# Kernel tuning notes

Measured on AMD Instinct MI355X. Metric: run time of the kernel, lower is better.

## Reference

```python
import jax, jax.numpy as jnp
import numpy as np

# ---- constants from conf ----
DT = 0.01
INIT_TAU = 0.5
MIN_TAU = 0.1
VTH = 1.0
VREST = 0.0
SLOPE = 25.0  # snntorch surrogate.fast_sigmoid default slope
IN, H1, H2, OUT = 700, 1024, 1024, 20
T, B = 100, 256

# fast-sigmoid surrogate: heaviside forward, 1/(1+slope|x|)^2 backward
@jax.custom_vjp
def spike_fn(x):
    return (x > 0).astype(x.dtype)

def _spike_fwd(x):
    return spike_fn(x), x

def _spike_bwd(x, g):
    return (g / (1.0 + SLOPE * jnp.abs(x)) ** 2,)

spike_fn.defvjp(_spike_fwd, _spike_bwd)

def lif_step(v, cur, w_tau):
    # per-neuron trainable time constant: tau = min_tau + sigmoid(w)
    tau = MIN_TAU + jax.nn.sigmoid(w_tau)
    v_new = v + (DT / tau) * (VREST - v + cur)
    s = spike_fn(v_new - VTH)
    v_reset = v_new * (1.0 - s) + VREST * s  # reset-to-zero mechanism
    return s, v_new, v_reset

def setup_inputs() -> dict:
    key = jax.random.key(0)
    ks = jax.random.split(key, 7)
    w_tau0 = float(np.log((INIT_TAU - MIN_TAU) / (1.0 - (INIT_TAU - MIN_TAU))))
    def lin(k, fan_in, fan_out):
        bound = 1.0 / np.sqrt(fan_in)
        kw, kb = jax.random.split(k)
        W = jax.random.uniform(kw, (fan_out, fan_in), jnp.float32, -bound, bound)
        b = jax.random.uniform(kb, (fan_out,), jnp.float32, -bound, bound)
        return W, b
    W1, b1 = lin(ks[0], IN, H1)
    W2, b2 = lin(ks[1], H1, H2)
    W3, b3 = lin(ks[2], H2, OUT)
    return {
        "s": jax.random.uniform(ks[3], (T, B, IN), jnp.float32),
        "W1": W1, "b1": b1, "wt1": jnp.full((H1,), w_tau0, jnp.float32),
        "W2": W2, "b2": b2, "wt2": jnp.full((H2,), w_tau0, jnp.float32),
        "W3": W3, "b3": b3, "wt3": jnp.full((OUT,), w_tau0, jnp.float32),
    }

def reference(s, W1, b1, wt1, W2, b2, wt2, W3, b3, wt3):
    Bq = s.shape[1]
    v0 = (jnp.full((Bq, H1), VREST, s.dtype),
          jnp.full((Bq, H2), VREST, s.dtype),
          jnp.full((Bq, OUT), VREST, s.dtype))

    def step(carry, st):
        v1, v2, v3 = carry
        s1, _, v1r = lif_step(v1, st @ W1.T + b1, wt1)
        s2, _, v2r = lif_step(v2, s1 @ W2.T + b2, wt2)
        s3, v3n, v3r = lif_step(v3, s2 @ W3.T + b3, wt3)
        return (v1r, v2r, v3r), (s3, v3n)

    _, (out_s, out_v) = jax.lax.scan(step, v0, s)
    return out_s, out_v  # [T,B,OUT] spikes and pre-reset membrane
```

## Files before the change

kernel.cpp:

```cpp
#include <hip/hip_runtime.h>

#define DT 0.01f
#define MIN_TAU 0.1f
#define VTH 1.0f
#define IN_DIM 700
#define H1 1024
#define H2 1024
#define OUT_DIM 20
#define T_STEPS 100
#define BATCH 256
#define M_ROWS (T_STEPS * BATCH)
#define KB_CNT 22
#define MT_CNT 1600
#define NT_CNT 64

typedef unsigned short u16;
typedef __attribute__((ext_vector_type(4))) float f32x4;
typedef __attribute__((ext_vector_type(8))) short short8;

__device__ __forceinline__ float bf2f(u16 u){ return __uint_as_float(((unsigned)u) << 16); }
__device__ __forceinline__ u16 f2bf(float f){
    unsigned x = __float_as_uint(f);
    return (u16)((x + 0x7fffu + ((x >> 16) & 1u)) >> 16);
}
template<bool ISBF>
__device__ __forceinline__ float ld1(const void* p, size_t i){
    return ISBF ? bf2f(((const u16*)p)[i]) : ((const float*)p)[i];
}

template<bool ISBF>
__global__ __launch_bounds__(256) void prep_tile(
    const void* __restrict__ Sraw, const void* __restrict__ W1raw,
    const void* __restrict__ b1raw, const void* __restrict__ wt1raw,
    u16* __restrict__ Stil, u16* __restrict__ Wtil, float* __restrict__ B1f)
{
    const u16* wt1u = (const u16*)wt1raw;
    if ((wt1u[0] == wt1u[1]) != ISBF) return;

    int u = blockIdx.x * 256 + threadIdx.x;
    const int SU = MT_CNT * KB_CNT * 64;
    const int WU = NT_CNT * KB_CNT * 64;
    if (u >= SU + WU){
        int i = u - SU - WU;
        B1f[i] = ld1<ISBF>(b1raw, i);
        return;
    }
    const void* src;
    u16* dst;
    int tile, lo;
    if (u < SU){ tile = u >> 6; lo = u & 63; src = Sraw;  dst = Stil; }
    else { int uu = u - SU; tile = uu >> 6; lo = uu & 63; src = W1raw; dst = Wtil; }
    const int rt = tile / KB_CNT, kb = tile - rt * KB_CNT;
    const int lr = lo >> 2, lg = lo & 3;
    const int row = rt * 16 + lr;
    const int k0 = kb * 32 + lg * 8;

    u16 out[8];
    if (k0 + 7 < IN_DIM){
        if (ISBF){
            const u16* p = (const u16*)src + (size_t)row * IN_DIM + k0;
            ushort4 q0 = *(const ushort4*)p, q1 = *(const ushort4*)(p + 4);
            out[0]=q0.x; out[1]=q0.y; out[2]=q0.z; out[3]=q0.w;
            out[4]=q1.x; out[5]=q1.y; out[6]=q1.z; out[7]=q1.w;
        } else {
            const float* p = (const float*)src + (size_t)row * IN_DIM + k0;
            float4 f0 = *(const float4*)p, f1 = *(const float4*)(p + 4);
            out[0]=f2bf(f0.x); out[1]=f2bf(f0.y); out[2]=f2bf(f0.z); out[3]=f2bf(f0.w);
            out[4]=f2bf(f1.x); out[5]=f2bf(f1.y); out[6]=f2bf(f1.z); out[7]=f2bf(f1.w);
        }
    } else {
        #pragma unroll
        for (int j = 0; j < 8; ++j){
            int k = k0 + j;
            out[j] = (k < IN_DIM) ? (ISBF ? ((const u16*)src)[(size_t)row * IN_DIM + k]
                                          : f2bf(((const float*)src)[(size_t)row * IN_DIM + k]))
                                  : (u16)0;
        }
    }
    *(short8*)&dst[(size_t)tile * 512 + lo * 8] = *(short8*)&out[0];
}

__global__ __launch_bounds__(512) void gemm256(
    const u16* __restrict__ Stil, const u16* __restrict__ Wtil,
    const float* __restrict__ B1f, u16* __restrict__ CUR1)
{
    __shared__ u16 Lb[2][24 * 512];
    const int bid = blockIdx.x;
    const int swz = (bid & 7) * 100 + (bid >> 3);
    const int mB = swz >> 3, nB = swz & 7;
    const int tid = threadIdx.x;
    const int lane = tid & 63, wv = tid >> 6;
    const int lr = lane & 15, lg = lane >> 4;
    const int loff = lr * 32 + lg * 8;
    const int wm = wv >> 1, wn = wv & 1;

    const int tgrp = tid >> 6;
    const int l16o = (tid & 63) * 8;
    const u16* pA0 = Stil + (size_t)(mB * 16 +     tgrp) * KB_CNT * 512 + l16o;
    const u16* pA1 = Stil + (size_t)(mB * 16 + 8 + tgrp) * KB_CNT * 512 + l16o;
    const u16* pB0 = Wtil + (size_t)(nB * 8  +     tgrp) * KB_CNT * 512 + l16o;
    const int d0 = tgrp * 512 + l16o;
    const int d1 = (8 + tgrp) * 512 + l16o;
    const int d2 = (16 + tgrp) * 512 + l16o;

    const int m0g = mB * 256 + wm * 64, n0g = nB * 128 + wn * 64;
    float bias[4];
    #pragma unroll
    for (int nf = 0; nf < 4; ++nf) bias[nf] = B1f[n0g + nf * 16 + lr];

    f32x4 acc[4][4];
    #pragma unroll
    for (int i = 0; i < 4; ++i)
        #pragma unroll
        for (int j = 0; j < 4; ++j) acc[i][j] = (f32x4){0.f, 0.f, 0.f, 0.f};

    short8 sA0 = *(const short8*)pA0;
    short8 sA1 = *(const short8*)pA1;
    short8 sB0 = *(const short8*)pB0;
    *(short8*)&Lb[0][d0] = sA0;
    *(short8*)&Lb[0][d1] = sA1;
    *(short8*)&Lb[0][d2] = sB0;
    __syncthreads();

    int cur = 0;
    #pragma unroll 1
    for (int kb = 0; kb < KB_CNT; ++kb){
        const bool more = (kb + 1) < KB_CNT;
        if (more){
            sA0 = *(const short8*)(pA0 + (kb + 1) * 512);
            sA1 = *(const short8*)(pA1 + (kb + 1) * 512);
            sB0 = *(const short8*)(pB0 + (kb + 1) * 512);
        }
        short8 af[4], bf[4];
        #pragma unroll
        for (int mf = 0; mf < 4; ++mf)
            af[mf] = *(const short8*)&Lb[cur][(wm * 4 + mf) * 512 + loff];
        #pragma unroll
        for (int nf = 0; nf < 4; ++nf)
            bf[nf] = *(const short8*)&Lb[cur][(16 + wn * 4 + nf) * 512 + loff];
        #pragma unroll
        for (int mf = 0; mf < 4; ++mf)
            #pragma unroll
            for (int nf = 0; nf < 4; ++nf)
                acc[mf][nf] = __builtin_amdgcn_mfma_f32_16x16x32_bf16(
                    af[mf], bf[nf], acc[mf][nf], 0, 0, 0);
        if (more){
            *(short8*)&Lb[cur ^ 1][d0] = sA0;
            *(short8*)&Lb[cur ^ 1][d1] = sA1;
            *(short8*)&Lb[cur ^ 1][d2] = sB0;
        }
        __syncthreads();
        cur ^= 1;
    }

    #pragma unroll
    for (int mf = 0; mf < 4; ++mf)
        #pragma unroll
        for (int nf = 0; nf < 4; ++nf)
            #pragma unroll
            for (int r = 0; r < 4; ++r)
                CUR1[(size_t)(m0g + mf*16 + lg*4 + r) * H1 + (n0g + nf*16 + lr)]
                    = f2bf(acc[mf][nf][r] + bias[nf]);
}

template<bool ISBF>
__global__ __launch_bounds__(64, 1) void scan_wave(
    const u16* __restrict__ CUR1,
    const void* __restrict__ wt1raw,
    const void* __restrict__ W2raw, const void* __restrict__ b2raw,
    const void* __restrict__ wt2raw,const void* __restrict__ W3raw,
    const void* __restrict__ b3raw, const void* __restrict__ wt3raw,
    void* __restrict__ outraw)
{
    const u16* wt1u = (const u16*)wt1raw;
    if ((wt1u[0] == wt1u[1]) != ISBF) return;

    const int b = blockIdx.x, lane = threadIdx.x;
    const int n0 = lane * 16;

    float v1[16], v2[16], kk1[16], kk2[16], b2f[16];
    #pragma unroll
    for (int r = 0; r < 16; ++r){
        kk1[r] = DT / (MIN_TAU + 1.f / (1.f + expf(-ld1<ISBF>(wt1raw, n0 + r))));
        kk2[r] = DT / (MIN_TAU + 1.f / (1.f + expf(-ld1<ISBF>(wt2raw, n0 + r))));
        b2f[r] = ld1<ISBF>(b2raw, n0 + r);
        v1[r] = 0.f; v2[r] = 0.f;
    }
    float v3 = 0.f, kk3 = 0.f, b3f = 0.f;
    if (lane < OUT_DIM){
        kk3 = DT / (MIN_TAU + 1.f / (1.f + expf(-ld1<ISBF>(wt3raw, lane))));
        b3f = ld1<ISBF>(b3raw, lane);
    }
    const size_t TBO = (size_t)T_STEPS * BATCH * OUT_DIM;
    const u16* cbase = CUR1 + (size_t)b * H1 + n0;
    const size_t tstride = (size_t)BATCH * H1;

    float rec_v[5];
    float rec_s[5];

    auto ldc = [&](int t, short8* dst){
        if (t < T_STEPS){
            const u16* p = cbase + (size_t)t * tstride;
            dst[0] = *(const short8*)p;
            dst[1] = *(const short8*)(p + 8);
        } else {
            dst[0] = (short8){0,0,0,0,0,0,0,0};
            dst[1] = (short8){0,0,0,0,0,0,0,0};
        }
    };

    auto do_step = [&](int s, short8 c0, short8 c1){
        #pragma unroll
        for (int r = 0; r < 16; ++r){
            u16 cu = (u16)(r < 8 ? c0[r] : c1[r - 8]);
            v1[r] = v1[r] + kk1[r] * (bf2f(cu) - v1[r]);
        }
        float mx1 = v1[0];
        #pragma unroll
        for (int r = 1; r < 16; ++r) mx1 = fmaxf(mx1, v1[r]);

        float cur3 = b3f;
        if (__any(mx1 > VTH)){
            unsigned m1 = 0u;
            #pragma unroll
            for (int r = 0; r < 16; ++r){
                bool sp = v1[r] > VTH;
                v1[r] = sp ? 0.f : v1[r];
                m1 |= sp ? (1u << r) : 0u;
            }
            unsigned long long bal1 = __ballot((int)(m1 != 0u));
            float cur2[16];
            #pragma unroll
            for (int r = 0; r < 16; ++r) cur2[r] = b2f[r];
            unsigned long long bb = bal1;
            while (bb){
                int L = __ffsll(bb) - 1; bb &= bb - 1;
                unsigned mk = __shfl(m1, L);
                while (mk){
                    int j = L * 16 + __ffs(mk) - 1; mk &= mk - 1;
                    #pragma unroll
                    for (int r = 0; r < 16; ++r)
                        cur2[r] += ld1<ISBF>(W2raw, (size_t)(n0 + r) * H1 + j);
                }
            }
            unsigned m2 = 0u;
            #pragma unroll
            for (int r = 0; r < 16; ++r){
                float vn = v2[r] + kk2[r] * (cur2[r] - v2[r]);
                bool sp = vn > VTH;
                v2[r] = sp ? 0.f : vn;
                m2 |= sp ? (1u << r) : 0u;
            }
            unsigned long long bal2 = __ballot((int)(m2 != 0u));
            unsigned long long b2b = bal2;
            while (b2b){
                int L = __ffsll(b2b) - 1; b2b &= b2b - 1;
                unsigned mk = __shfl(m2, L);
                while (mk){
                    int j = L * 16 + __ffs(mk) - 1; mk &= mk - 1;
                    float w = (lane < OUT_DIM)
                            ? ld1<ISBF>(W3raw, (size_t)lane * H2 + j) : 0.f;
                    cur3 += w;
                }
            }
        } else {
            #pragma unroll
            for (int r = 0; r < 16; ++r)
                v2[r] = v2[r] + kk2[r] * (b2f[r] - v2[r]);
            float mx2 = v2[0];
            #pragma unroll
            for (int r = 1; r < 16; ++r) mx2 = fmaxf(mx2, v2[r]);
            if (__any(mx2 > VTH)){
                unsigned m2 = 0u;
                #pragma unroll
                for (int r = 0; r < 16; ++r){
                    bool sp = v2[r] > VTH;
                    v2[r] = sp ? 0.f : v2[r];
                    m2 |= sp ? (1u << r) : 0u;
                }
                unsigned long long bal2 = __ballot((int)(m2 != 0u));
                unsigned long long b2b = bal2;
                while (b2b){
                    int L = __ffsll(b2b) - 1; b2b &= b2b - 1;
                    unsigned mk = __shfl(m2, L);
                    while (mk){
                        int j = L * 16 + __ffs(mk) - 1; mk &= mk - 1;
                        float w = (lane < OUT_DIM)
                                ? ld1<ISBF>(W3raw, (size_t)lane * H2 + j) : 0.f;
                        cur3 += w;
                    }
                }
            }
        }

        float vn3 = v3 + kk3 * (cur3 - v3);
        bool sp3 = vn3 > VTH;
        rec_s[s] = sp3 ? 1.f : 0.f;
        rec_v[s] = vn3;
        v3 = sp3 ? 0.f : vn3;
    };

    auto flush = [&](int tb){
        if (lane < OUT_DIM){
            #pragma unroll
            for (int s = 0; s < 5; ++s){
                int t = tb + s;
                size_t o = ((size_t)t * BATCH + b) * OUT_DIM + lane;
                if (ISBF){
                    u16* ob = (u16*)outraw;
                    ob[o] = (rec_s[s] != 0.f) ? (u16)0x3F80 : (u16)0;
                    ob[TBO + o] = f2bf(rec_v[s]);
                } else {
                    float* of = (float*)outraw;
                    of[o] = rec_s[s];
                    of[TBO + o] = rec_v[s];
                }
            }
        }
    };

    short8 pA[5][2], pB[5][2];
    #pragma unroll
    for (int s = 0; s < 5; ++s) ldc(s, pA[s]);

    #pragma unroll 1
    for (int g2 = 0; g2 < 10; ++g2){
        const int tb = g2 * 10;
        #pragma unroll
        for (int s = 0; s < 5; ++s) ldc(tb + 5 + s, pB[s]);
        #pragma unroll
        for (int s = 0; s < 5; ++s) do_step(s, pA[s][0], pA[s][1]);
        flush(tb);
        #pragma unroll
        for (int s = 0; s < 5; ++s) ldc(tb + 10 + s, pA[s]);
        #pragma unroll
        for (int s = 0; s < 5; ++s) do_step(s, pB[s][0], pB[s][1]);
        flush(tb + 5);
    }
}

template<bool ISBF>
__global__ __launch_bounds__(256) void gemm_cur1(
    const void* __restrict__ Sraw, const void* __restrict__ W1raw,
    const void* __restrict__ wt1raw, u16* __restrict__ CUR1)
{
    const u16* wt1u = (const u16*)wt1raw;
    if ((wt1u[0] == wt1u[1]) != ISBF) return;

    __shared__ u16 lds[2][2][128][40];
    const int tid = threadIdx.x;
    const int n0 = blockIdx.x * 128;
    const int m0 = blockIdx.y * 128;
    const int row = tid >> 1, half = tid & 1;
    const int lane = tid & 63, wv = tid >> 6;
    const int lr = lane & 15, lg = lane >> 4;
    const int wm = wv >> 1, wn = wv & 1;

    float4  fa[4], fb[4];
    ushort4 ha[4], hb[4];

    auto load_seg = [&](const void* base, int grow, int kb, float4* fr, ushort4* hr){
        const int cg0 = kb * 32 + half * 16;
        #pragma unroll
        for (int q = 0; q < 4; ++q){
            const int cg = cg0 + q * 4;
            if (ISBF){
                const u16* p = (const u16*)base + (size_t)grow * IN_DIM + cg;
                ushort4 v = make_ushort4(0,0,0,0);
                if (cg + 3 < IN_DIM) v = *(const ushort4*)p;
                else {
                    if (cg     < IN_DIM) v.x = p[0];
                    if (cg + 1 < IN_DIM) v.y = p[1];
                    if (cg + 2 < IN_DIM) v.z = p[2];
                    if (cg + 3 < IN_DIM) v.w = p[3];
                }
                hr[q] = v;
            } else {
                const float* p = (const float*)base + (size_t)grow * IN_DIM + cg;
                float4 f = make_float4(0,0,0,0);
                if (cg + 3 < IN_DIM) f = *(const float4*)p;
                else {
                    if (cg     < IN_DIM) f.x = p[0];
                    if (cg + 1 < IN_DIM) f.y = p[1];
                    if (cg + 2 < IN_DIM) f.z = p[2];
                    if (cg + 3 < IN_DIM) f.w = p[3];
                }
                fr[q] = f;
            }
        }
    };
    auto load_ab = [&](int kb){
        load_seg(Sraw,  m0 + row, kb, fa, ha);
        load_seg(W1raw, n0 + row, kb, fb, hb);
    };
    auto cvt_store = [&](int buf){
        u16 ta[16], tb[16];
        #pragma unroll
        for (int q = 0; q < 4; ++q){
            if (ISBF){
                ta[q*4+0]=ha[q].x; ta[q*4+1]=ha[q].y; ta[q*4+2]=ha[q].z; ta[q*4+3]=ha[q].w;
                tb[q*4+0]=hb[q].x; tb[q*4+1]=hb[q].y; tb[q*4+2]=hb[q].z; tb[q*4+3]=hb[q].w;
            } else {
                ta[q*4+0]=f2bf(fa[q].x); ta[q*4+1]=f2bf(fa[q].y);
                ta[q*4+2]=f2bf(fa[q].z); ta[q*4+3]=f2bf(fa[q].w);
                tb[q*4+0]=f2bf(fb[q].x); tb[q*4+1]=f2bf(fb[q].y);
                tb[q*4+2]=f2bf(fb[q].z); tb[q*4+3]=f2bf(fb[q].w);
            }
        }
        *(short8*)&lds[0][buf][row][half*16    ] = *(short8*)&ta[0];
        *(short8*)&lds[0][buf][row][half*16 + 8] = *(short8*)&ta[8];
        *(short8*)&lds[1][buf][row][half*16    ] = *(short8*)&tb[0];
        *(short8*)&lds[1][buf][row][half*16 + 8] = *(short8*)&tb[8];
    };

    f32x4 acc[4][4];
    #pragma unroll
    for (int i = 0; i < 4; ++i)
        #pragma unroll
        for (int j = 0; j < 4; ++j) acc[i][j] = (f32x4){0.f,0.f,0.f,0.f};

    load_ab(0);
    cvt_store(0);
    __syncthreads();

    for (int kb = 0; kb < 22; ++kb){
        const int cur = kb & 1;
        const bool more = (kb + 1) < 22;
        if (more) load_ab(kb + 1);

        short8 afr[4], bfr[4];
        #pragma unroll
        for (int mf = 0; mf < 4; ++mf)
            afr[mf] = *(const short8*)&lds[0][cur][wm*64 + mf*16 + lr][lg*8];
        #pragma unroll
        for (int nf = 0; nf < 4; ++nf)
            bfr[nf] = *(const short8*)&lds[1][cur][wn*64 + nf*16 + lr][lg*8];
        #pragma unroll
        for (int mf = 0; mf < 4; ++mf)
            #pragma unroll
            for (int nf = 0; nf < 4; ++nf)
                acc[mf][nf] = __builtin_amdgcn_mfma_f32_16x16x32_bf16(
                    afr[mf], bfr[nf], acc[mf][nf], 0, 0, 0);

        if (more) cvt_store(cur ^ 1);
        __syncthreads();
    }

    u16 (*Cep)[136] = (u16(*)[136])&lds[0][0][0][0];
    #pragma unroll
    for (int mf = 0; mf < 4; ++mf)
        #pragma unroll
        for (int nf = 0; nf < 4; ++nf)
            #pragma unroll
            for (int r = 0; r < 4; ++r)
                Cep[wm*64 + mf*16 + lg*4 + r][wn*64 + nf*16 + lr] = f2bf(acc[mf][nf][r]);
    __syncthreads();
    #pragma unroll
    for (int q = 0; q < 8; ++q){
        int idx = q * 256 + tid;
        int r = idx >> 4, c = (idx & 15) * 8;
        *(short8*)&CUR1[(size_t)(m0 + r) * H1 + n0 + c] = *(short8*)&Cep[r][c];
    }
}

template<bool ISBF>
__global__ __launch_bounds__(256) void scan_cur(
    const u16* __restrict__ CUR1,
    const void* __restrict__ b1raw, const void* __restrict__ wt1raw,
    const void* __restrict__ W2raw, const void* __restrict__ b2raw,
    const void* __restrict__ wt2raw,const void* __restrict__ W3raw,
    const void* __restrict__ b3raw, const void* __restrict__ wt3raw,
    void* __restrict__ outraw)
{
    const u16* wt1u = (const u16*)wt1raw;
    if ((wt1u[0] == wt1u[1]) != ISBF) return;

    const int b = blockIdx.x, tid = threadIdx.x;
    __shared__ __align__(16) unsigned mask1[2][32], mask2[2][32];
    __shared__ __align__(16) unsigned wflag1[2][4], wflag2[2][4];

    float v1[4] = {0,0,0,0}, v2[4] = {0,0,0,0};
    float kk1[4], kk2[4], b1f[4], b2f[4];
    #pragma unroll
    for (int c = 0; c < 4; ++c){
        int n = tid * 4 + c;
        kk1[c] = DT / (MIN_TAU + 1.f / (1.f + expf(-ld1<ISBF>(wt1raw, n))));
        kk2[c] = DT / (MIN_TAU + 1.f / (1.f + expf(-ld1<ISBF>(wt2raw, n))));
        b1f[c] = ld1<ISBF>(b1raw, n);
        b2f[c] = ld1<ISBF>(b2raw, n);
    }
    float v3 = 0.f, kk3 = 0.f, b3f = 0.f;
    if (tid < OUT_DIM){
        kk3 = DT / (MIN_TAU + 1.f / (1.f + expf(-ld1<ISBF>(wt3raw, tid))));
        b3f = ld1<ISBF>(b3raw, tid);
    }
    const size_t TBO = (size_t)T_STEPS * BATCH * OUT_DIM;

    if (tid < 32){ mask1[0][tid] = 0u; mask2[0][tid] = 0u; }
    if (tid < 4){ wflag1[0][tid] = 0u; wflag2[0][tid] = 0u; }

    auto ld_cur = [&](int t) -> ushort4 {
        if (t < T_STEPS)
            return *(const ushort4*)&CUR1[((size_t)t * BATCH + b) * H1 + tid * 4];
        return make_ushort4(0, 0, 0, 0);
    };

    auto do_step = [&](int t, ushort4 cu){
        const int p = t & 1;
        unsigned nib = 0u;
        u16 ca[4] = {cu.x, cu.y, cu.z, cu.w};
        #pragma unroll
        for (int c = 0; c < 4; ++c){
            float cur1 = bf2f(ca[c]) + b1f[c];
            float vn = v1[c] + kk1[c] * (cur1 - v1[c]);
            bool sp = vn > VTH;
            v1[c] = sp ? 0.f : vn;
            nib |= sp ? (1u << c) : 0u;
        }
        if (nib) atomicOr(&mask1[p][tid >> 3], nib << ((tid * 4) & 31));
        bool wany1 = __any((int)(nib != 0u));
        if ((tid & 63) == 0) wflag1[p][tid >> 6] = wany1 ? 1u : 0u;
        __syncthreads();

        uint4 f1 = *(const uint4*)&wflag1[p][0];
        float cur2[4] = {b2f[0], b2f[1], b2f[2], b2f[3]};
        if (f1.x | f1.y | f1.z | f1.w){
            for (int w = 0; w < 32; ++w){
                unsigned bits = mask1[p][w];
                while (bits){
                    int j = (w << 5) + __ffs(bits) - 1;
                    bits &= bits - 1;
                    #pragma unroll
                    for (int c = 0; c < 4; ++c)
                        cur2[c] += ld1<ISBF>(W2raw, (size_t)(tid * 4 + c) * H1 + j);
                }
            }
        }
        unsigned nib2 = 0u;
        #pragma unroll
        for (int c = 0; c < 4; ++c){
            float vn = v2[c] + kk2[c] * (cur2[c] - v2[c]);
            bool sp = vn > VTH;
            v2[c] = sp ? 0.f : vn;
            nib2 |= sp ? (1u << c) : 0u;
        }
        if (nib2) atomicOr(&mask2[p][tid >> 3], nib2 << ((tid * 4) & 31));
        bool wany2 = __any((int)(nib2 != 0u));
        if ((tid & 63) == 0) wflag2[p][tid >> 6] = wany2 ? 1u : 0u;
        if (tid >= 128 && tid < 160) mask1[p ^ 1][tid - 128] = 0u;
        if (tid >= 160 && tid < 164) wflag1[p ^ 1][tid - 160] = 0u;
        __syncthreads();

        if (tid < OUT_DIM){
            uint4 f2 = *(const uint4*)&wflag2[p][0];
            float cur3 = b3f;
            if (f2.x | f2.y | f2.z | f2.w){
                for (int w = 0; w < 32; ++w){
                    unsigned bits = mask2[p][w];
                    while (bits){
                        int j = (w << 5) + __ffs(bits) - 1;
                        bits &= bits - 1;
                        cur3 += ld1<ISBF>(W3raw, (size_t)tid * H2 + j);
                    }
                }
            }
            float vn = v3 + kk3 * (cur3 - v3);
            bool sp = vn > VTH;
            size_t o = ((size_t)t * BATCH + b) * OUT_DIM + tid;
            if (ISBF){
                u16* ob = (u16*)outraw;
                ob[o] = sp ? (u16)0x3F80 : (u16)0;
                ob[TBO + o] = f2bf(vn);
            } else {
                float* of = (float*)outraw;
                of[o] = sp ? 1.f : 0.f;
                of[TBO + o] = vn;
            }
            v3 = sp ? 0.f : vn;
        }
        if (tid >= 32 && tid < 64) mask2[p ^ 1][tid - 32] = 0u;
        if (tid >= 64 && tid < 68) wflag2[p ^ 1][tid - 64] = 0u;
        __syncthreads();
    };

    ushort4 pfA[10], pfB[10];
    #pragma unroll
    for (int s = 0; s < 10; ++s) pfA[s] = ld_cur(s);
    __syncthreads();

    #pragma unroll 1
    for (int g2 = 0; g2 < 5; ++g2){
        const int tb = g2 * 20;
        #pragma unroll
        for (int s = 0; s < 10; ++s) pfB[s] = ld_cur(tb + 10 + s);
        #pragma unroll
        for (int s = 0; s < 10; ++s) do_step(tb + s, pfA[s]);
        #pragma unroll
        for (int s = 0; s < 10; ++s) pfA[s] = ld_cur(tb + 20 + s);
        #pragma unroll
        for (int s = 0; s < 10; ++s) do_step(tb + 10 + s, pfB[s]);
    }
}

extern "C" void kernel_launch(void* const* d_in, const int* in_sizes, int n_in,
                              void* d_out, int out_size, void* d_ws, size_t ws_size,
                              hipStream_t stream)
{
    (void)in_sizes; (void)n_in; (void)out_size;
    const size_t STIL_B = (size_t)MT_CNT * KB_CNT * 512 * 2;
    const size_t WTIL_B = (size_t)NT_CNT * KB_CNT * 512 * 2;
    const size_t B1F_B  = 4096;
    const size_t CUR1_B = (size_t)M_ROWS * H1 * 2;
    const size_t NEED_T1 = STIL_B + WTIL_B + B1F_B + CUR1_B;

    if (ws_size >= NEED_T1){
        u16*   Stil = (u16*)d_ws;
        u16*   Wtil = (u16*)((char*)d_ws + STIL_B);
        float* B1f  = (float*)((char*)d_ws + STIL_B + WTIL_B);
        u16*   CUR1 = (u16*)((char*)d_ws + STIL_B + WTIL_B + B1F_B);
        const int units = (MT_CNT + NT_CNT) * KB_CNT * 64 + 1024;
        hipLaunchKernelGGL(prep_tile<false>, dim3(units / 256), dim3(256), 0, stream,
                           d_in[0], d_in[1], d_in[2], d_in[3], Stil, Wtil, B1f);
        hipLaunchKernelGGL(prep_tile<true>,  dim3(units / 256), dim3(256), 0, stream,
                           d_in[0], d_in[1], d_in[2], d_in[3], Stil, Wtil, B1f);
        hipLaunchKernelGGL(gemm256, dim3(800), dim3(512), 0, stream,
                           Stil, Wtil, B1f, CUR1);
        hipLaunchKernelGGL(scan_wave<false>, dim3(BATCH), dim3(64), 0, stream,
                           CUR1, d_in[3], d_in[4], d_in[5], d_in[6],
                           d_in[7], d_in[8], d_in[9], d_out);
        hipLaunchKernelGGL(scan_wave<true>,  dim3(BATCH), dim3(64), 0, stream,
                           CUR1, d_in[3], d_in[4], d_in[5], d_in[6],
                           d_in[7], d_in[8], d_in[9], d_out);
    } else if (ws_size >= CUR1_B){
        u16* CUR1 = (u16*)d_ws;
        hipLaunchKernelGGL(gemm_cur1<false>, dim3(8, 200), dim3(256), 0, stream,
                           d_in[0], d_in[1], d_in[3], CUR1);
        hipLaunchKernelGGL(gemm_cur1<true>,  dim3(8, 200), dim3(256), 0, stream,
                           d_in[0], d_in[1], d_in[3], CUR1);
        hipLaunchKernelGGL(scan_cur<false>, dim3(BATCH), dim3(256), 0, stream,
                           CUR1, d_in[2], d_in[3], d_in[4], d_in[5], d_in[6],
                           d_in[7], d_in[8], d_in[9], d_out);
        hipLaunchKernelGGL(scan_cur<true>,  dim3(BATCH), dim3(256), 0, stream,
                           CUR1, d_in[2], d_in[3], d_in[4], d_in[5], d_in[6],
                           d_in[7], d_in[8], d_in[9], d_out);
    }
}
```

Measured before the change: 105.5 us.

## Merge dtype-templated launches, make LDS fragment reads contiguous, deepen GEMM prefetch

```diff
diff --git a/kernel.cpp b/kernel.cpp
--- a/kernel.cpp
+++ b/kernel.cpp
@@ -23,26 +23,28 @@
     unsigned x = __float_as_uint(f);
     return (u16)((x + 0x7fffu + ((x >> 16) & 1u)) >> 16);
 }
+__device__ __forceinline__ float ldr(bool isbf, const void* p, size_t i){
+    return isbf ? bf2f(((const u16*)p)[i]) : ((const float*)p)[i];
+}
 template<bool ISBF>
 __device__ __forceinline__ float ld1(const void* p, size_t i){
     return ISBF ? bf2f(((const u16*)p)[i]) : ((const float*)p)[i];
 }
 
-template<bool ISBF>
 __global__ __launch_bounds__(256) void prep_tile(
     const void* __restrict__ Sraw, const void* __restrict__ W1raw,
     const void* __restrict__ b1raw, const void* __restrict__ wt1raw,
     u16* __restrict__ Stil, u16* __restrict__ Wtil, float* __restrict__ B1f)
 {
     const u16* wt1u = (const u16*)wt1raw;
-    if ((wt1u[0] == wt1u[1]) != ISBF) return;
+    const bool isbf = (wt1u[0] == wt1u[1]);
 
     int u = blockIdx.x * 256 + threadIdx.x;
     const int SU = MT_CNT * KB_CNT * 64;
     const int WU = NT_CNT * KB_CNT * 64;
     if (u >= SU + WU){
         int i = u - SU - WU;
-        B1f[i] = ld1<ISBF>(b1raw, i);
+        B1f[i] = ldr(isbf, b1raw, i);
         return;
     }
     const void* src;
@@ -51,13 +53,13 @@
     if (u < SU){ tile = u >> 6; lo = u & 63; src = Sraw;  dst = Stil; }
     else { int uu = u - SU; tile = uu >> 6; lo = uu & 63; src = W1raw; dst = Wtil; }
     const int rt = tile / KB_CNT, kb = tile - rt * KB_CNT;
-    const int lr = lo >> 2, lg = lo & 3;
+    const int lr = lo & 15, lg = lo >> 4;
     const int row = rt * 16 + lr;
     const int k0 = kb * 32 + lg * 8;
 
     u16 out[8];
     if (k0 + 7 < IN_DIM){
-        if (ISBF){
+        if (isbf){
             const u16* p = (const u16*)src + (size_t)row * IN_DIM + k0;
             ushort4 q0 = *(const ushort4*)p, q1 = *(const ushort4*)(p + 4);
             out[0]=q0.x; out[1]=q0.y; out[2]=q0.z; out[3]=q0.w;
@@ -72,7 +74,7 @@
         #pragma unroll
         for (int j = 0; j < 8; ++j){
             int k = k0 + j;
-            out[j] = (k < IN_DIM) ? (ISBF ? ((const u16*)src)[(size_t)row * IN_DIM + k]
+            out[j] = (k < IN_DIM) ? (isbf ? ((const u16*)src)[(size_t)row * IN_DIM + k]
                                           : f2bf(((const float*)src)[(size_t)row * IN_DIM + k]))
                                   : (u16)0;
         }
@@ -91,7 +93,7 @@
     const int tid = threadIdx.x;
     const int lane = tid & 63, wv = tid >> 6;
     const int lr = lane & 15, lg = lane >> 4;
-    const int loff = lr * 32 + lg * 8;
+    const int loff = lane * 8;
     const int wm = wv >> 1, wn = wv & 1;
 
     const int tgrp = tid >> 6;
@@ -114,43 +116,61 @@
         #pragma unroll
         for (int j = 0; j < 4; ++j) acc[i][j] = (f32x4){0.f, 0.f, 0.f, 0.f};
 
-    short8 sA0 = *(const short8*)pA0;
-    short8 sA1 = *(const short8*)pA1;
-    short8 sB0 = *(const short8*)pB0;
-    *(short8*)&Lb[0][d0] = sA0;
-    *(short8*)&Lb[0][d1] = sA1;
-    *(short8*)&Lb[0][d2] = sB0;
+    short8 eA0 = *(const short8*)pA0;
+    short8 eA1 = *(const short8*)pA1;
+    short8 eB0 = *(const short8*)pB0;
+    *(short8*)&Lb[0][d0] = eA0;
+    *(short8*)&Lb[0][d1] = eA1;
+    *(short8*)&Lb[0][d2] = eB0;
+    short8 oA0 = *(const short8*)(pA0 + 512);
+    short8 oA1 = *(const short8*)(pA1 + 512);
+    short8 oB0 = *(const short8*)(pB0 + 512);
     __syncthreads();
 
-    int cur = 0;
-    #pragma unroll 1
-    for (int kb = 0; kb < KB_CNT; ++kb){
-        const bool more = (kb + 1) < KB_CNT;
-        if (more){
-            sA0 = *(const short8*)(pA0 + (kb + 1) * 512);
-            sA1 = *(const short8*)(pA1 + (kb + 1) * 512);
-            sB0 = *(const short8*)(pB0 + (kb + 1) * 512);
-        }
+    auto compute = [&](int buf){
         short8 af[4], bf[4];
         #pragma unroll
         for (int mf = 0; mf < 4; ++mf)
-            af[mf] = *(const short8*)&Lb[cur][(wm * 4 + mf) * 512 + loff];
+            af[mf] = *(const short8*)&Lb[buf][(wm * 4 + mf) * 512 + loff];
         #pragma unroll
         for (int nf = 0; nf < 4; ++nf)
-            bf[nf] = *(const short8*)&Lb[cur][(16 + wn * 4 + nf) * 512 + loff];
+            bf[nf] = *(const short8*)&Lb[buf][(16 + wn * 4 + nf) * 512 + loff];
         #pragma unroll
         for (int mf = 0; mf < 4; ++mf)
             #pragma unroll
             for (int nf = 0; nf < 4; ++nf)
                 acc[mf][nf] = __builtin_amdgcn_mfma_f32_16x16x32_bf16(
                     af[mf], bf[nf], acc[mf][nf], 0, 0, 0);
-        if (more){
-            *(short8*)&Lb[cur ^ 1][d0] = sA0;
-            *(short8*)&Lb[cur ^ 1][d1] = sA1;
-            *(short8*)&Lb[cur ^ 1][d2] = sB0;
-        }
+    };
+
+    #pragma unroll 1
+    for (int kb = 0; kb < KB_CNT; kb += 2){
+        const bool m2 = (kb + 2) < KB_CNT;
+        if (m2){
+            eA0 = *(const short8*)(pA0 + (kb + 2) * 512);
+            eA1 = *(const short8*)(pA1 + (kb + 2) * 512);
+            eB0 = *(const short8*)(pB0 + (kb + 2) * 512);
+        }
+        compute(0);
+        *(short8*)&Lb[1][d0] = oA0;
+        *(short8*)&Lb[1][d1] = oA1;
+        *(short8*)&Lb[1][d2] = oB0;
         __syncthreads();
-        cur ^= 1;
+
+        if (m2){
+            if ((kb + 3) < KB_CNT){
+                oA0 = *(const short8*)(pA0 + (kb + 3) * 512);
+                oA1 = *(const short8*)(pA1 + (kb + 3) * 512);
+                oB0 = *(const short8*)(pB0 + (kb + 3) * 512);
+            }
+            compute(1);
+            *(short8*)&Lb[0][d0] = eA0;
+            *(short8*)&Lb[0][d1] = eA1;
+            *(short8*)&Lb[0][d2] = eB0;
+            __syncthreads();
+        } else {
+            compute(1);
+        }
     }
 
     #pragma unroll
@@ -163,7 +183,6 @@
                     = f2bf(acc[mf][nf][r] + bias[nf]);
 }
 
-template<bool ISBF>
 __global__ __launch_bounds__(64, 1) void scan_wave(
     const u16* __restrict__ CUR1,
     const void* __restrict__ wt1raw,
@@ -173,7 +192,7 @@
     void* __restrict__ outraw)
 {
     const u16* wt1u = (const u16*)wt1raw;
-    if ((wt1u[0] == wt1u[1]) != ISBF) return;
+    const bool isbf = (wt1u[0] == wt1u[1]);
 
     const int b = blockIdx.x, lane = threadIdx.x;
     const int n0 = lane * 16;
@@ -181,15 +200,15 @@
     float v1[16], v2[16], kk1[16], kk2[16], b2f[16];
     #pragma unroll
     for (int r = 0; r < 16; ++r){
-        kk1[r] = DT / (MIN_TAU + 1.f / (1.f + expf(-ld1<ISBF>(wt1raw, n0 + r))));
-        kk2[r] = DT / (MIN_TAU + 1.f / (1.f + expf(-ld1<ISBF>(wt2raw, n0 + r))));
-        b2f[r] = ld1<ISBF>(b2raw, n0 + r);
+        kk1[r] = DT / (MIN_TAU + 1.f / (1.f + expf(-ldr(isbf, wt1raw, n0 + r))));
+        kk2[r] = DT / (MIN_TAU + 1.f / (1.f + expf(-ldr(isbf, wt2raw, n0 + r))));
+        b2f[r] = ldr(isbf, b2raw, n0 + r);
         v1[r] = 0.f; v2[r] = 0.f;
     }
     float v3 = 0.f, kk3 = 0.f, b3f = 0.f;
     if (lane < OUT_DIM){
-        kk3 = DT / (MIN_TAU + 1.f / (1.f + expf(-ld1<ISBF>(wt3raw, lane))));
-        b3f = ld1<ISBF>(b3raw, lane);
+        kk3 = DT / (MIN_TAU + 1.f / (1.f + expf(-ldr(isbf, wt3raw, lane))));
+        b3f = ldr(isbf, b3raw, lane);
     }
     const size_t TBO = (size_t)T_STEPS * BATCH * OUT_DIM;
     const u16* cbase = CUR1 + (size_t)b * H1 + n0;
@@ -240,7 +259,7 @@
                     int j = L * 16 + __ffs(mk) - 1; mk &= mk - 1;
                     #pragma unroll
                     for (int r = 0; r < 16; ++r)
-                        cur2[r] += ld1<ISBF>(W2raw, (size_t)(n0 + r) * H1 + j);
+                        cur2[r] += ldr(isbf, W2raw, (size_t)(n0 + r) * H1 + j);
                 }
             }
             unsigned m2 = 0u;
@@ -259,7 +278,7 @@
                 while (mk){
                     int j = L * 16 + __ffs(mk) - 1; mk &= mk - 1;
                     float w = (lane < OUT_DIM)
-                            ? ld1<ISBF>(W3raw, (size_t)lane * H2 + j) : 0.f;
+                            ? ldr(isbf, W3raw, (size_t)lane * H2 + j) : 0.f;
                     cur3 += w;
                 }
             }
@@ -286,7 +305,7 @@
                     while (mk){
                         int j = L * 16 + __ffs(mk) - 1; mk &= mk - 1;
                         float w = (lane < OUT_DIM)
-                                ? ld1<ISBF>(W3raw, (size_t)lane * H2 + j) : 0.f;
+                                ? ldr(isbf, W3raw, (size_t)lane * H2 + j) : 0.f;
                         cur3 += w;
                     }
                 }
@@ -306,7 +325,7 @@
             for (int s = 0; s < 5; ++s){
                 int t = tb + s;
                 size_t o = ((size_t)t * BATCH + b) * OUT_DIM + lane;
-                if (ISBF){
+                if (isbf){
                     u16* ob = (u16*)outraw;
                     ob[o] = (rec_s[s] != 0.f) ? (u16)0x3F80 : (u16)0;
                     ob[TBO + o] = f2bf(rec_v[s]);
@@ -619,16 +638,11 @@
         float* B1f  = (float*)((char*)d_ws + STIL_B + WTIL_B);
         u16*   CUR1 = (u16*)((char*)d_ws + STIL_B + WTIL_B + B1F_B);
         const int units = (MT_CNT + NT_CNT) * KB_CNT * 64 + 1024;
-        hipLaunchKernelGGL(prep_tile<false>, dim3(units / 256), dim3(256), 0, stream,
-                           d_in[0], d_in[1], d_in[2], d_in[3], Stil, Wtil, B1f);
-        hipLaunchKernelGGL(prep_tile<true>,  dim3(units / 256), dim3(256), 0, stream,
+        hipLaunchKernelGGL(prep_tile, dim3(units / 256), dim3(256), 0, stream,
                            d_in[0], d_in[1], d_in[2], d_in[3], Stil, Wtil, B1f);
         hipLaunchKernelGGL(gemm256, dim3(800), dim3(512), 0, stream,
                            Stil, Wtil, B1f, CUR1);
-        hipLaunchKernelGGL(scan_wave<false>, dim3(BATCH), dim3(64), 0, stream,
-                           CUR1, d_in[3], d_in[4], d_in[5], d_in[6],
-                           d_in[7], d_in[8], d_in[9], d_out);
-        hipLaunchKernelGGL(scan_wave<true>,  dim3(BATCH), dim3(64), 0, stream,
+        hipLaunchKernelGGL(scan_wave, dim3(BATCH), dim3(64), 0, stream,
                            CUR1, d_in[3], d_in[4], d_in[5], d_in[6],
                            d_in[7], d_in[8], d_in[9], d_out);
     } else if (ws_size >= CUR1_B){
```

New measurement: 119.5 us. 1.13x slower.
